# Kernel optimization log

Measured on AMD Instinct MI355X. Metric: run time of the kernel, lower is better.

Reference implementation:

```python
import jax, jax.numpy as jnp
import numpy as np

N, H, W, C, G, K = 8, 64, 64, 128, 8, 3
GC = C // G          # group channels = 16
P = K * K            # 9 sampling points
PAD = DIL = STRIDE = 1
OS = 1.0             # offset_scale
EPS = 1e-6
H_IN, W_IN = H + 2 * PAD, W + 2 * PAD


def _grid_sample_nhwc(img, grid):
    # img: (B, Hi, Wi, Cc) ; grid: (B, L, Pp, 2) in [-1,1]
    # bilinear, padding_mode='zeros', align_corners=False (matches F.grid_sample)
    B, Hi, Wi, Cc = img.shape
    gx = (grid[..., 0] + 1.0) * (Wi * 0.5) - 0.5
    gy = (grid[..., 1] + 1.0) * (Hi * 0.5) - 0.5
    x0 = jnp.floor(gx)
    y0 = jnp.floor(gy)
    wx1 = gx - x0
    wy1 = gy - y0
    b = jnp.arange(B).reshape(B, 1, 1)

    def tap(xi, yi, wgt):
        valid = (xi >= 0) & (xi <= Wi - 1) & (yi >= 0) & (yi <= Hi - 1)
        xc = jnp.clip(xi, 0, Wi - 1).astype(jnp.int32)
        yc = jnp.clip(yi, 0, Hi - 1).astype(jnp.int32)
        return img[b, yc, xc] * (wgt * valid)[..., None]

    return (tap(x0, y0, (1 - wx1) * (1 - wy1))
            + tap(x0 + 1, y0, wx1 * (1 - wy1))
            + tap(x0, y0 + 1, (1 - wx1) * wy1)
            + tap(x0 + 1, y0 + 1, wx1 * wy1))


def _forward(x, w_in, b_in, dw_w, dw_b, ln_g, ln_b, w_off, b_off, w_msk, b_msk, w_out, b_out):
    n = x.shape[0]
    x_proj = x @ w_in + b_in                                  # input_proj (n,H,W,C)
    # dw_conv: depthwise 3x3 -> LayerNorm(channels_last) -> GELU
    x1 = jax.lax.conv_general_dilated(
        x, dw_w, (1, 1), [((K - 1) // 2,) * 2] * 2,
        dimension_numbers=('NHWC', 'HWIO', 'NHWC'), feature_group_count=C) + dw_b
    mu = jnp.mean(x1, -1, keepdims=True)
    var = jnp.mean((x1 - mu) ** 2, -1, keepdims=True)
    x1 = (x1 - mu) * jax.lax.rsqrt(var + EPS) * ln_g + ln_b
    x1 = jax.nn.gelu(x1, approximate=False)
    offset = x1 @ w_off + b_off                               # (n,H,W,G*P*2)
    mask = jax.nn.softmax((x1 @ w_msk + b_msk).reshape(n, H, W, G, P), axis=-1)
    # reference points on the padded input (pixel-center, normalized)
    ry = (DIL * (K - 1) // 2 + 0.5 + jnp.arange(H, dtype=jnp.float32) * STRIDE) / H_IN
    rx = (DIL * (K - 1) // 2 + 0.5 + jnp.arange(W, dtype=jnp.float32) * STRIDE) / W_IN
    ref = jnp.stack([jnp.broadcast_to(rx[None, :], (H, W)),
                     jnp.broadcast_to(ry[:, None], (H, W))], -1)      # (H,W,2) = (x,y)
    # dilation kernel grid, x-major flatten (matches torch meshgrid indexing='ij')
    ks = jnp.arange(K, dtype=jnp.float32) * DIL - DIL * (K - 1) // 2
    gxk, gyk = jnp.meshgrid(ks, ks, indexing='ij')
    pts = jnp.stack([gxk / W_IN, gyk / H_IN], -1).reshape(P, 2)
    pts = jnp.tile(pts, (G, 1))                                       # (G*P,2), group-major
    loc = (ref[:, :, None, :] + pts[None, None, :, :] * OS).reshape(1, H, W, G * P * 2)
    snorm = jnp.tile(jnp.array([W_IN, H_IN], jnp.float32), G * P)     # [w,h,w,h,...]
    loc = loc + offset * OS / snorm
    grids = (2.0 * loc - 1.0).reshape(n, H * W, G, P, 2)
    grids = grids.transpose(0, 2, 1, 3, 4).reshape(n * G, H * W, P, 2)
    x_pad = jnp.pad(x_proj, ((0, 0), (PAD, PAD), (PAD, PAD), (0, 0)))
    img = x_pad.reshape(n, H_IN, W_IN, G, GC).transpose(0, 3, 1, 2, 4).reshape(n * G, H_IN, W_IN, GC)
    sampled = _grid_sample_nhwc(img, grids)                            # (n*G, HW, P, GC)
    m = mask.reshape(n, H * W, G, P).transpose(0, 2, 1, 3).reshape(n * G, H * W, P)
    out = (sampled * m[..., None]).sum(2)                              # (n*G, HW, GC)
    out = out.reshape(n, G, H * W, GC).transpose(0, 2, 1, 3).reshape(n, H, W, C)
    return out @ w_out + b_out                                         # output_proj


def setup_inputs():
    key = jax.random.key(0)
    k = jax.random.split(key, 8)
    s = 0.02
    f = jnp.float32
    return {
        'x': jax.random.normal(k[0], (N, H, W, C), f),
        'w_in': jax.random.normal(k[1], (C, C), f) * (1.0 / np.sqrt(C)),
        'b_in': jnp.zeros((C,), f),
        'dw_w': jax.random.normal(k[2], (K, K, 1, C), f) * s,
        'dw_b': jnp.zeros((C,), f),
        'ln_g': jnp.ones((C,), f),
        'ln_b': jnp.zeros((C,), f),
        'w_off': jax.random.normal(k[3], (C, G * P * 2), f) * s,
        'b_off': jax.random.normal(k[4], (G * P * 2,), f) * s,
        'w_msk': jax.random.normal(k[5], (C, G * P), f) * s,
        'b_msk': jnp.zeros((G * P,), f),
        'w_out': jax.random.normal(k[6], (C, C), f) * (1.0 / np.sqrt(C)),
        'b_out': jnp.zeros((C,), f),
    }


def reference(x, w_in, b_in, dw_w, dw_b, ln_g, ln_b, w_off, b_off, w_msk, b_msk, w_out, b_out):
    return _forward(x, w_in, b_in, dw_w, dw_b, ln_g, ln_b, w_off, b_off, w_msk, b_msk, w_out, b_out)
```

## Files before the change

### kernel.cpp

```cpp
#include <hip/hip_runtime.h>
#include <math.h>

#define NB 8
#define H 64
#define W 64
#define C 128
#define G 8
#define GC 16
#define P 9
#define NPIX (NB * H * W)
#define N_OFF 144
#define N_MSK 72
#define PXB 32
#define RECW 232
#define PK_IN_ELEMS   (8 * 4 * 64 * 8)
#define PK_COMB_ELEMS (14 * 4 * 64 * 8)
#define PK_OUT_ELEMS  (8 * 4 * 64 * 8)

using bf16x8 = __attribute__((ext_vector_type(8))) short;
using f32x4  = __attribute__((ext_vector_type(4))) float;
using u32x4  = __attribute__((ext_vector_type(4))) unsigned;

__device__ __forceinline__ short f2bf(float f) {
    union { float fv; unsigned u; } v; v.fv = f;
    unsigned r = v.u + 0x7fffu + ((v.u >> 16) & 1u);
    return (short)(r >> 16);
}

__global__ __launch_bounds__(256) void k_pack(
    const float* __restrict__ w_in, const float* __restrict__ w_off,
    const float* __restrict__ w_msk, const float* __restrict__ w_out,
    short* __restrict__ pk_in, short* __restrict__ pk_comb, short* __restrict__ pk_out)
{
    const int tid = blockIdx.x * 256 + threadIdx.x;
    int p, which;
    if (tid < PK_IN_ELEMS) { p = tid; which = 0; }
    else if (tid < PK_IN_ELEMS + PK_COMB_ELEMS) { p = tid - PK_IN_ELEMS; which = 1; }
    else if (tid < PK_IN_ELEMS + PK_COMB_ELEMS + PK_OUT_ELEMS) { p = tid - PK_IN_ELEMS - PK_COMB_ELEMS; which = 2; }
    else return;
    const int e = p & 7, lane = (p >> 3) & 63, kt = (p >> 9) & 3, nt = p >> 11;
    const int k = kt * 32 + (lane >> 4) * 8 + e;
    const int n = nt * 16 + (lane & 15);
    float v;
    if (which == 0) {
        v = w_in[k * C + n];
        pk_in[p] = f2bf(v);
    } else if (which == 1) {
        if (n < N_OFF) v = w_off[k * N_OFF + n];
        else if (n < N_OFF + N_MSK) v = w_msk[k * N_MSK + (n - N_OFF)];
        else v = 0.f;
        pk_comb[p] = f2bf(v);
    } else {
        v = w_out[k * C + n];
        pk_out[p] = f2bf(v);
    }
}

__global__ __launch_bounds__(256, 2) void k_fm(
    const float* __restrict__ x, const float* __restrict__ dw_w,
    const float* __restrict__ dw_b, const float* __restrict__ ln_g,
    const float* __restrict__ ln_b, const short* __restrict__ pk_in,
    const float* __restrict__ b_in, const short* __restrict__ pk_comb,
    const float* __restrict__ b_off, const float* __restrict__ b_msk,
    unsigned short* __restrict__ xproj, float* __restrict__ out)
{
    __shared__ __align__(16) short xa[PXB * C];
    __shared__ __align__(16) short x1s[PXB * C];
    __shared__ unsigned short recs[PXB * RECW];

    const int t = threadIdx.x;
    const int n = blockIdx.x & 7;
    const int local = blockIdx.x >> 3;
    const int y = local >> 1;
    const int xb = (local & 1) * PXB;
    const int gpix0 = (n * H + y) * W + xb;

    const int px = t >> 3;
    const int c8 = t & 7;
    const int cb = c8 * 4;
    const int gpx = gpix0 + px;
    const int sw = (px & 7) << 4;

    float a[16];
    #pragma unroll
    for (int q = 0; q < 4; ++q) {
        f32x4 v = *(const f32x4*)(dw_b + cb + q * 32);
        #pragma unroll
        for (int e = 0; e < 4; ++e) a[q * 4 + e] = v[e];
    }
    #pragma unroll
    for (int ky = 0; ky < 3; ++ky) {
        const int yy = y + ky - 1;
        if (yy < 0 || yy >= H) continue;
        #pragma unroll
        for (int kx = 0; kx < 3; ++kx) {
            const int xx = xb + px + kx - 1;
            if (xx < 0 || xx >= W) continue;
            const float* xp = x + ((size_t)(n * H + yy) * W + xx) * C;
            const float* wp = dw_w + (ky * 3 + kx) * C;
            #pragma unroll
            for (int q = 0; q < 4; ++q) {
                f32x4 xv = *(const f32x4*)(xp + cb + q * 32);
                f32x4 wv = *(const f32x4*)(wp + cb + q * 32);
                #pragma unroll
                for (int e = 0; e < 4; ++e)
                    a[q * 4 + e] = fmaf(xv[e], wv[e], a[q * 4 + e]);
            }
        }
    }
    {
        const float* cp = x + (size_t)gpx * C;
        #pragma unroll
        for (int q = 0; q < 4; ++q) {
            f32x4 v = *(const f32x4*)(cp + cb + q * 32);
            const unsigned lo = ((unsigned)(unsigned short)f2bf(v[0])) |
                                (((unsigned)(unsigned short)f2bf(v[1])) << 16);
            const unsigned hi = ((unsigned)(unsigned short)f2bf(v[2])) |
                                (((unsigned)(unsigned short)f2bf(v[3])) << 16);
            *(unsigned long long*)((char*)xa + px * 256 + ((cb * 2 + q * 64) ^ sw)) =
                ((unsigned long long)hi << 32) | lo;
        }
    }
    float mu, rsg;
    {
        float s = 0.f, sq = 0.f;
        #pragma unroll
        for (int cc = 0; cc < 16; ++cc) { s += a[cc]; sq = fmaf(a[cc], a[cc], sq); }
        #pragma unroll
        for (int d = 1; d < 8; d <<= 1) {
            s += __shfl_xor(s, d);
            sq += __shfl_xor(sq, d);
        }
        mu = s * (1.f / C);
        const float va = sq * (1.f / C) - mu * mu;
        rsg = rsqrtf(va + 1e-6f);
    }
    #pragma unroll
    for (int q = 0; q < 4; ++q) {
        f32x4 gv = *(const f32x4*)(ln_g + cb + q * 32);
        f32x4 bv = *(const f32x4*)(ln_b + cb + q * 32);
        unsigned short h4[4];
        #pragma unroll
        for (int e = 0; e < 4; ++e) {
            float v = (a[q * 4 + e] - mu) * rsg * gv[e] + bv[e];
            h4[e] = (unsigned short)f2bf(v * 0.5f * (1.f + erff(v * 0.70710678118654752f)));
        }
        const unsigned lo = ((unsigned)h4[0]) | (((unsigned)h4[1]) << 16);
        const unsigned hi = ((unsigned)h4[2]) | (((unsigned)h4[3]) << 16);
        *(unsigned long long*)((char*)x1s + px * 256 + ((cb * 2 + q * 64) ^ sw)) =
            ((unsigned long long)hi << 32) | lo;
    }
    __syncthreads();

    {
        const int w = t >> 6, l = t & 63;
        const int swA = (l & 7) << 4;
        bf16x8 aA[2][4], aB[2][4];
        #pragma unroll
        for (int mt = 0; mt < 2; ++mt) {
            const int m = mt * 16 + (l & 15);
            #pragma unroll
            for (int kt = 0; kt < 4; ++kt) {
                const int byte = m * 256 + ((kt * 64 + (l >> 4) * 16) ^ swA);
                aA[mt][kt] = *(const bf16x8*)((char*)xa + byte);
                aB[mt][kt] = *(const bf16x8*)((char*)x1s + byte);
            }
        }
        #pragma unroll
        for (int i = 0; i < 2; ++i) {
            const int nt = w + i * 4;
            bf16x8 bf[4];
            const short* bp = pk_in + nt * 2048 + l * 8;
            #pragma unroll
            for (int kt = 0; kt < 4; ++kt) bf[kt] = *(const bf16x8*)(bp + kt * 512);
            const float bias = b_in[nt * 16 + (l & 15)];
            #pragma unroll
            for (int mt = 0; mt < 2; ++mt) {
                f32x4 acc = {0.f, 0.f, 0.f, 0.f};
                #pragma unroll
                for (int kt = 0; kt < 4; ++kt)
                    acc = __builtin_amdgcn_mfma_f32_16x16x32_bf16(aA[mt][kt], bf[kt], acc, 0, 0, 0);
                const int prow = gpix0 + mt * 16 + (l >> 4) * 4;
                #pragma unroll
                for (int r = 0; r < 4; ++r)
                    xproj[(size_t)(nt * NPIX + prow + r) * 16 + (l & 15)] =
                        (unsigned short)f2bf(acc[r] + bias);
            }
        }
        #pragma unroll
        for (int i = 0; i < 4; ++i) {
            const int nt = w + i * 4;
            if (nt < 14) {
                bf16x8 bf[4];
                const short* bp = pk_comb + nt * 2048 + l * 8;
                #pragma unroll
                for (int kt = 0; kt < 4; ++kt) bf[kt] = *(const bf16x8*)(bp + kt * 512);
                const int col = nt * 16 + (l & 15);
                int dcol = col;
                float bias = 0.f;
                bool valid = true;
                if (col < N_OFF) bias = b_off[col];
                else {
                    const int cm = col - N_OFF;
                    if (cm < N_MSK) {
                        const int g = (cm * 57) >> 9;
                        dcol = 144 + g * 10 + (cm - 9 * g);
                        bias = b_msk[cm];
                    } else valid = false;
                }
                #pragma unroll
                for (int mt = 0; mt < 2; ++mt) {
                    f32x4 acc = {0.f, 0.f, 0.f, 0.f};
                    #pragma unroll
                    for (int kt = 0; kt < 4; ++kt)
                        acc = __builtin_amdgcn_mfma_f32_16x16x32_bf16(aB[mt][kt], bf[kt], acc, 0, 0, 0);
                    if (valid) {
                        const int pr0 = mt * 16 + (l >> 4) * 4;
                        #pragma unroll
                        for (int r = 0; r < 4; ++r)
                            recs[(pr0 + r) * RECW + dcol] = (unsigned short)f2bf(acc[r] + bias);
                    }
                }
            }
        }
    }
    __syncthreads();

    {
        const int spx = t >> 3, g = t & 7;
        unsigned short* row = recs + spx * RECW + 144 + g * 10;
        float lg[P];
        #pragma unroll
        for (int p = 0; p < P; ++p) lg[p] = __uint_as_float(((unsigned)row[p]) << 16);
        float mx = lg[0];
        #pragma unroll
        for (int p2 = 1; p2 < P; ++p2) mx = fmaxf(mx, lg[p2]);
        float e[P], s = 0.f;
        #pragma unroll
        for (int p2 = 0; p2 < P; ++p2) { e[p2] = expf(lg[p2] - mx); s += e[p2]; }
        const float inv = 1.0f / s;
        #pragma unroll
        for (int p2 = 0; p2 < P; ++p2) row[p2] = (unsigned short)f2bf(e[p2] * inv);
    }
    __syncthreads();

    {
        const int spx = t >> 3, q0 = t & 7;
        const char* srcL = (const char*)recs + spx * (RECW * 2);
        char* dst = (char*)out + (size_t)(gpix0 + spx) * 512;
        #pragma unroll
        for (int h = 0; h < 4; ++h) {
            const int q = q0 + h * 8;
            if (q < 28)
                *(bf16x8*)(dst + q * 16) = *(const bf16x8*)(srcL + q * 16);
        }
    }
}

#define PADX 41
__global__ __launch_bounds__(256, 2) void k_samp(
    const unsigned short* __restrict__ xproj, const short* __restrict__ pk_out,
    const float* __restrict__ b_out, float* __restrict__ out)
{
    __shared__ __align__(16) short smp[PXB * C];
    __shared__ __align__(16) u32x4 win[2 * 4 * 5 * PADX];

    const int t = threadIdx.x;
    const int n = blockIdx.x & 7;
    const int local = blockIdx.x >> 3;
    const int y = local >> 1;
    const int xb = (local & 1) * PXB;
    const int gpix0 = (n * H + y) * W + xb;
    const int imgbase = n * (H * W);

    const int spx = t & 31;
    const int gl = (t >> 5) & 3;
    const int half = t >> 7;
    const int xabs = xb + spx;
    const int swz = (spx & 7) << 4;
    const unsigned* slot = (const unsigned*)((const char*)out +
                           (size_t)(gpix0 + spx) * 512);

    for (int f = 0; f < 2; ++f) {
        const int g = f * 4 + gl;

        float cf[25];
        #pragma unroll
        for (int i = 0; i < 25; ++i) cf[i] = 0.f;
        float amax = 0.f;
        {
            u32x4 a0 = *(const u32x4*)(slot + g * 9);
            u32x4 a1 = *(const u32x4*)(slot + g * 9 + 4);
            const unsigned ov8 = slot[g * 9 + 8];
            u32x4 b0 = *(const u32x4*)(slot + 72 + 5 * g);
            const unsigned pb4 = slot[72 + 5 * g + 4];
            #pragma unroll
            for (int p = 0; p < P; ++p) {
                const unsigned ovp = (p < 4) ? a0[p & 3] : (p < 8) ? a1[p & 3] : ov8;
                const unsigned pu = (p < 8) ? b0[p >> 1] : pb4;
                const float m = (p & 1) ? __uint_as_float(pu & 0xffff0000u)
                                        : __uint_as_float(pu << 16);
                const float ox = __uint_as_float(ovp << 16);
                const float oy = __uint_as_float(ovp & 0xffff0000u);
                amax = fmaxf(amax, fmaxf(fabsf(ox), fabsf(oy)));
                const float fx = floorf(ox);
                const float fy = floorf(oy);
                const float wx = ox - fx, wy = oy - fy;
                const bool lox = fx < -0.5f;
                const bool loy = fy < -0.5f;
                const float wc0 = lox ? (1.f - wx) : 0.f;
                const float wc1 = lox ? wx : (1.f - wx);
                const float wc2 = lox ? 0.f : wx;
                const float wr0 = loy ? (1.f - wy) : 0.f;
                const float wr1 = loy ? wy : (1.f - wy);
                const float wr2 = loy ? 0.f : wy;
                const float mr0 = m * wr0, mr1 = m * wr1, mr2 = m * wr2;
                const int dxp = p / 3 - 1, dyp = p % 3 - 1;
                const int base = (dyp + 1) * 5 + (dxp + 1);
                cf[base + 0]  = fmaf(wc0, mr0, cf[base + 0]);
                cf[base + 1]  = fmaf(wc1, mr0, cf[base + 1]);
                cf[base + 2]  = fmaf(wc2, mr0, cf[base + 2]);
                cf[base + 5]  = fmaf(wc0, mr1, cf[base + 5]);
                cf[base + 6]  = fmaf(wc1, mr1, cf[base + 6]);
                cf[base + 7]  = fmaf(wc2, mr1, cf[base + 7]);
                cf[base + 10] = fmaf(wc0, mr2, cf[base + 10]);
                cf[base + 11] = fmaf(wc1, mr2, cf[base + 11]);
                cf[base + 12] = fmaf(wc2, mr2, cf[base + 12]);
            }
        }
        #pragma unroll
        for (int j = 0; j < 5; ++j) {
            const int xc = xabs + j - 2;
            if (!((xc >= 0) & (xc < W))) {
                #pragma unroll
                for (int i = 0; i < 5; ++i) cf[i * 5 + j] = 0.f;
            }
        }
        #pragma unroll
        for (int i = 0; i < 5; ++i) {
            const int yc = y + i - 2;
            if (!((yc >= 0) & (yc < H))) {
                #pragma unroll
                for (int j = 0; j < 5; ++j) cf[i * 5 + j] = 0.f;
            }
        }
        __syncthreads();

        for (int e = t; e < 1600; e += 256) {
            const int uh = e & 1;
            const int v = e >> 1;
            const int xs = v % 40;
            const int q2 = v / 40;
            const int rs = q2 % 5;
            const int gs = q2 / 5;
            const int row = min(max(y - 2 + rs, 0), H - 1);
            const int col = min(max(xb - 4 + xs, 0), W - 1);
            win[((uh * 4 + gs) * 5 + rs) * PADX + xs] =
                *(const u32x4*)(xproj +
                    ((size_t)((f * 4 + gs) * NPIX + imgbase + row * W + col)) * 16 + uh * 8);
        }
        __syncthreads();

        {
            float acc[8];
            #pragma unroll
            for (int q = 0; q < 8; ++q) acc[q] = 0.f;
            if (amax < 1.0f) {
                const u32x4* wb = win + (half * 4 + gl) * 5 * PADX + spx + 2;
                #pragma unroll
                for (int rr = 0; rr < 5; ++rr) {
                    #pragma unroll
                    for (int cc = 0; cc < 5; ++cc) {
                        const float c = cf[rr * 5 + cc];
                        const u32x4 v = wb[rr * PADX + cc];
                        #pragma unroll
                        for (int e = 0; e < 4; ++e) {
                            acc[2 * e]     = fmaf(c, __uint_as_float(v[e] << 16), acc[2 * e]);
                            acc[2 * e + 1] = fmaf(c, __uint_as_float(v[e] & 0xffff0000u), acc[2 * e + 1]);
                        }
                    }
                }
            } else {
                const u32x4* plane4 = (const u32x4*)(xproj + (size_t)(g * NPIX + imgbase) * 16);
                for (int p = 0; p < P; ++p) {
                    const unsigned ovp = slot[g * 9 + p];
                    const unsigned pu = slot[72 + 5 * g + (p >> 1)];
                    const float m = (p & 1) ? __uint_as_float(pu & 0xffff0000u)
                                            : __uint_as_float(pu << 16);
                    const float ux = (float)(xabs + (p / 3) - 1) + __uint_as_float(ovp << 16);
                    const float uy = (float)(y + (p % 3) - 1) + __uint_as_float(ovp & 0xffff0000u);
                    const float fx = floorf(ux), fy = floorf(uy);
                    const float wx = ux - fx, wy = uy - fy;
                    const int x0 = (int)fx, y0 = (int)fy;
                    float w4[4];
                    w4[0] = m * (1.f - wx) * (1.f - wy);
                    w4[1] = m * wx * (1.f - wy);
                    w4[2] = m * (1.f - wx) * wy;
                    w4[3] = m * wx * wy;
                    if (!((x0 >= 0) & (x0 < W)))       { w4[0] = 0.f; w4[2] = 0.f; }
                    if (!((x0 >= -1) & (x0 < W - 1)))  { w4[1] = 0.f; w4[3] = 0.f; }
                    if (!((y0 >= 0) & (y0 < H)))       { w4[0] = 0.f; w4[1] = 0.f; }
                    if (!((y0 >= -1) & (y0 < H - 1)))  { w4[2] = 0.f; w4[3] = 0.f; }
                    const int xc[2] = { min(max(x0, 0), W - 1), min(max(x0 + 1, 0), W - 1) };
                    const int yc[2] = { min(max(y0, 0), H - 1), min(max(y0 + 1, 0), H - 1) };
                    for (int cn = 0; cn < 4; ++cn) {
                        const float wgt = w4[cn];
                        if (wgt == 0.f) continue;
                        const u32x4 v = plane4[(size_t)(yc[cn >> 1] * W + xc[cn & 1]) * 2 + half];
                        #pragma unroll
                        for (int e = 0; e < 4; ++e) {
                            acc[2 * e]     = fmaf(wgt, __uint_as_float(v[e] << 16), acc[2 * e]);
                            acc[2 * e + 1] = fmaf(wgt, __uint_as_float(v[e] & 0xffff0000u), acc[2 * e + 1]);
                        }
                    }
                }
            }
            bf16x8 pk;
            #pragma unroll
            for (int e = 0; e < 8; ++e) pk[e] = f2bf(acc[e]);
            *(bf16x8*)((char*)smp + spx * 256 + ((g * 32 + half * 16) ^ swz)) = pk;
        }
    }
    __syncthreads();

    {
        const int w = t >> 6, l = t & 63;
        const int swA = (l & 7) << 4;
        bf16x8 aS[2][4];
        #pragma unroll
        for (int mt = 0; mt < 2; ++mt) {
            const int m = mt * 16 + (l & 15);
            #pragma unroll
            for (int kt = 0; kt < 4; ++kt)
                aS[mt][kt] = *(const bf16x8*)((char*)smp + m * 256 +
                                              ((kt * 64 + (l >> 4) * 16) ^ swA));
        }
        #pragma unroll
        for (int i = 0; i < 2; ++i) {
            const int nt = w + i * 4;
            bf16x8 bf[4];
            const short* bp = pk_out + nt * 2048 + l * 8;
            #pragma unroll
            for (int kt = 0; kt < 4; ++kt) bf[kt] = *(const bf16x8*)(bp + kt * 512);
            const float bias = b_out[nt * 16 + (l & 15)];
            #pragma unroll
            for (int mt = 0; mt < 2; ++mt) {
                f32x4 acc2 = {0.f, 0.f, 0.f, 0.f};
                #pragma unroll
                for (int kt = 0; kt < 4; ++kt)
                    acc2 = __builtin_amdgcn_mfma_f32_16x16x32_bf16(aS[mt][kt], bf[kt], acc2, 0, 0, 0);
                const int row0 = gpix0 + mt * 16 + (l >> 4) * 4;
                #pragma unroll
                for (int r = 0; r < 4; ++r)
                    out[(size_t)(row0 + r) * C + nt * 16 + (l & 15)] = acc2[r] + bias;
            }
        }
    }
}

extern "C" void kernel_launch(void* const* d_in, const int* in_sizes, int n_in,
                              void* d_out, int out_size, void* d_ws, size_t ws_size,
                              hipStream_t stream)
{
    const float* x     = (const float*)d_in[0];
    const float* w_in  = (const float*)d_in[1];
    const float* b_in  = (const float*)d_in[2];
    const float* dw_w  = (const float*)d_in[3];
    const float* dw_b  = (const float*)d_in[4];
    const float* ln_g  = (const float*)d_in[5];
    const float* ln_b  = (const float*)d_in[6];
    const float* w_off = (const float*)d_in[7];
    const float* b_off = (const float*)d_in[8];
    const float* w_msk = (const float*)d_in[9];
    const float* b_msk = (const float*)d_in[10];
    const float* w_out = (const float*)d_in[11];
    const float* b_out = (const float*)d_in[12];

    short* pk_in   = (short*)d_ws;
    short* pk_comb = pk_in + PK_IN_ELEMS;
    short* pk_out  = pk_comb + PK_COMB_ELEMS;
    unsigned short* xproj = (unsigned short*)(pk_out + PK_OUT_ELEMS);
    float* out     = (float*)d_out;

    hipLaunchKernelGGL(k_pack, dim3(240), dim3(256), 0, stream,
                       w_in, w_off, w_msk, w_out, pk_in, pk_comb, pk_out);
    hipLaunchKernelGGL(k_fm, dim3(NPIX / PXB), dim3(256), 0, stream,
                       x, dw_w, dw_b, ln_g, ln_b, pk_in, b_in,
                       pk_comb, b_off, b_msk, xproj, out);
    hipLaunchKernelGGL(k_samp, dim3(NPIX / PXB), dim3(256), 0, stream,
                       xproj, pk_out, b_out, out);
}
```

Measured before the change: 50.46 us.

## Split input projection into front kernel and fuse offset/mask with sampling and output

```diff
diff --git a/kernel.cpp b/kernel.cpp
--- a/kernel.cpp
+++ b/kernel.cpp
@@ -56,18 +56,10 @@
     }
 }
 
-__global__ __launch_bounds__(256, 2) void k_fm(
-    const float* __restrict__ x, const float* __restrict__ dw_w,
-    const float* __restrict__ dw_b, const float* __restrict__ ln_g,
-    const float* __restrict__ ln_b, const short* __restrict__ pk_in,
-    const float* __restrict__ b_in, const short* __restrict__ pk_comb,
-    const float* __restrict__ b_off, const float* __restrict__ b_msk,
-    unsigned short* __restrict__ xproj, float* __restrict__ out)
+__global__ __launch_bounds__(256, 2) void k_front(
+    const float* __restrict__ x, const short* __restrict__ pk_in,
+    const float* __restrict__ b_in, unsigned short* __restrict__ xproj)
 {
-    __shared__ __align__(16) short xa[PXB * C];
-    __shared__ __align__(16) short x1s[PXB * C];
-    __shared__ unsigned short recs[PXB * RECW];
-
     const int t = threadIdx.x;
     const int n = blockIdx.x & 7;
     const int local = blockIdx.x >> 3;
@@ -75,10 +67,67 @@
     const int xb = (local & 1) * PXB;
     const int gpix0 = (n * H + y) * W + xb;
 
+    const int w = t >> 6, l = t & 63;
+    bf16x8 aA[2][4];
+    #pragma unroll
+    for (int mt = 0; mt < 2; ++mt) {
+        const int m = mt * 16 + (l & 15);
+        const float* rp = x + (size_t)(gpix0 + m) * C + (l >> 4) * 8;
+        #pragma unroll
+        for (int kt = 0; kt < 4; ++kt) {
+            f32x4 v0 = *(const f32x4*)(rp + kt * 32);
+            f32x4 v1 = *(const f32x4*)(rp + kt * 32 + 4);
+            bf16x8 pk;
+            #pragma unroll
+            for (int e = 0; e < 4; ++e) { pk[e] = f2bf(v0[e]); pk[4 + e] = f2bf(v1[e]); }
+            aA[mt][kt] = pk;
+        }
+    }
+    #pragma unroll
+    for (int i = 0; i < 2; ++i) {
+        const int nt = w + i * 4;
+        bf16x8 bf[4];
+        const short* bp = pk_in + nt * 2048 + l * 8;
+        #pragma unroll
+        for (int kt = 0; kt < 4; ++kt) bf[kt] = *(const bf16x8*)(bp + kt * 512);
+        const float bias = b_in[nt * 16 + (l & 15)];
+        #pragma unroll
+        for (int mt = 0; mt < 2; ++mt) {
+            f32x4 acc = {0.f, 0.f, 0.f, 0.f};
+            #pragma unroll
+            for (int kt = 0; kt < 4; ++kt)
+                acc = __builtin_amdgcn_mfma_f32_16x16x32_bf16(aA[mt][kt], bf[kt], acc, 0, 0, 0);
+            const int prow = gpix0 + mt * 16 + (l >> 4) * 4;
+            #pragma unroll
+            for (int r = 0; r < 4; ++r)
+                xproj[(size_t)(nt * NPIX + prow + r) * 16 + (l & 15)] =
+                    (unsigned short)f2bf(acc[r] + bias);
+        }
+    }
+}
+
+__global__ __launch_bounds__(256, 2) void k_back(
+    const float* __restrict__ x, const float* __restrict__ dw_w,
+    const float* __restrict__ dw_b, const float* __restrict__ ln_g,
+    const float* __restrict__ ln_b, const short* __restrict__ pk_comb,
+    const float* __restrict__ b_off, const float* __restrict__ b_msk,
+    const unsigned short* __restrict__ xproj, const short* __restrict__ pk_out,
+    const float* __restrict__ b_out, float* __restrict__ out)
+{
+    __shared__ __align__(16) short buf0[PXB * C];
+    __shared__ unsigned short recs[PXB * RECW];
+
+    const int t = threadIdx.x;
+    const int n = blockIdx.x & 7;
+    const int local = blockIdx.x >> 3;
+    const int y = local >> 1;
+    const int xb = (local & 1) * PXB;
+    const int gpix0 = (n * H + y) * W + xb;
+    const int imgbase = n * (H * W);
+
     const int px = t >> 3;
     const int c8 = t & 7;
     const int cb = c8 * 4;
-    const int gpx = gpix0 + px;
     const int sw = (px & 7) << 4;
 
     float a[16];
@@ -108,19 +157,6 @@
             }
         }
     }
-    {
-        const float* cp = x + (size_t)gpx * C;
-        #pragma unroll
-        for (int q = 0; q < 4; ++q) {
-            f32x4 v = *(const f32x4*)(cp + cb + q * 32);
-            const unsigned lo = ((unsigned)(unsigned short)f2bf(v[0])) |
-                                (((unsigned)(unsigned short)f2bf(v[1])) << 16);
-            const unsigned hi = ((unsigned)(unsigned short)f2bf(v[2])) |
-                                (((unsigned)(unsigned short)f2bf(v[3])) << 16);
-            *(unsigned long long*)((char*)xa + px * 256 + ((cb * 2 + q * 64) ^ sw)) =
-                ((unsigned long long)hi << 32) | lo;
-        }
-    }
     float mu, rsg;
     {
         float s = 0.f, sq = 0.f;
@@ -131,8 +167,8 @@
             s += __shfl_xor(s, d);
             sq += __shfl_xor(sq, d);
         }
-        mu = s * (1.f / C);
-        const float va = sq * (1.f / C) - mu * mu;
+        mu = s * (1.0f / C);
+        const float va = sq * (1.0f / C) - mu * mu;
         rsg = rsqrtf(va + 1e-6f);
     }
     #pragma unroll
@@ -147,7 +183,7 @@
         }
         const unsigned lo = ((unsigned)h4[0]) | (((unsigned)h4[1]) << 16);
         const unsigned hi = ((unsigned)h4[2]) | (((unsigned)h4[3]) << 16);
-        *(unsigned long long*)((char*)x1s + px * 256 + ((cb * 2 + q * 64) ^ sw)) =
+        *(unsigned long long*)((char*)buf0 + px * 256 + ((cb * 2 + q * 64) ^ sw)) =
             ((unsigned long long)hi << 32) | lo;
     }
     __syncthreads();
@@ -155,37 +191,14 @@
     {
         const int w = t >> 6, l = t & 63;
         const int swA = (l & 7) << 4;
-        bf16x8 aA[2][4], aB[2][4];
+        bf16x8 aB[2][4];
         #pragma unroll
         for (int mt = 0; mt < 2; ++mt) {
             const int m = mt * 16 + (l & 15);
             #pragma unroll
-            for (int kt = 0; kt < 4; ++kt) {
-                const int byte = m * 256 + ((kt * 64 + (l >> 4) * 16) ^ swA);
-                aA[mt][kt] = *(const bf16x8*)((char*)xa + byte);
-                aB[mt][kt] = *(const bf16x8*)((char*)x1s + byte);
-            }
-        }
-        #pragma unroll
-        for (int i = 0; i < 2; ++i) {
-            const int nt = w + i * 4;
-            bf16x8 bf[4];
-            const short* bp = pk_in + nt * 2048 + l * 8;
-            #pragma unroll
-            for (int kt = 0; kt < 4; ++kt) bf[kt] = *(const bf16x8*)(bp + kt * 512);
-            const float bias = b_in[nt * 16 + (l & 15)];
-            #pragma unroll
-            for (int mt = 0; mt < 2; ++mt) {
-                f32x4 acc = {0.f, 0.f, 0.f, 0.f};
-                #pragma unroll
-                for (int kt = 0; kt < 4; ++kt)
-                    acc = __builtin_amdgcn_mfma_f32_16x16x32_bf16(aA[mt][kt], bf[kt], acc, 0, 0, 0);
-                const int prow = gpix0 + mt * 16 + (l >> 4) * 4;
-                #pragma unroll
-                for (int r = 0; r < 4; ++r)
-                    xproj[(size_t)(nt * NPIX + prow + r) * 16 + (l & 15)] =
-                        (unsigned short)f2bf(acc[r] + bias);
-            }
+            for (int kt = 0; kt < 4; ++kt)
+                aB[mt][kt] = *(const bf16x8*)((char*)buf0 + m * 256 +
+                                              ((kt * 64 + (l >> 4) * 16) ^ swA));
         }
         #pragma unroll
         for (int i = 0; i < 4; ++i) {
@@ -245,88 +258,45 @@
     __syncthreads();
 
     {
-        const int spx = t >> 3, q0 = t & 7;
-        const char* srcL = (const char*)recs + spx * (RECW * 2);
-        char* dst = (char*)out + (size_t)(gpix0 + spx) * 512;
-        #pragma unroll
-        for (int h = 0; h < 4; ++h) {
-            const int q = q0 + h * 8;
-            if (q < 28)
-                *(bf16x8*)(dst + q * 16) = *(const bf16x8*)(srcL + q * 16);
-        }
-    }
-}
-
-#define PADX 41
-__global__ __launch_bounds__(256, 2) void k_samp(
-    const unsigned short* __restrict__ xproj, const short* __restrict__ pk_out,
-    const float* __restrict__ b_out, float* __restrict__ out)
-{
-    __shared__ __align__(16) short smp[PXB * C];
-    __shared__ __align__(16) u32x4 win[2 * 4 * 5 * PADX];
-
-    const int t = threadIdx.x;
-    const int n = blockIdx.x & 7;
-    const int local = blockIdx.x >> 3;
-    const int y = local >> 1;
-    const int xb = (local & 1) * PXB;
-    const int gpix0 = (n * H + y) * W + xb;
-    const int imgbase = n * (H * W);
-
-    const int spx = t & 31;
-    const int gl = (t >> 5) & 3;
-    const int half = t >> 7;
-    const int xabs = xb + spx;
-    const int swz = (spx & 7) << 4;
-    const unsigned* slot = (const unsigned*)((const char*)out +
-                           (size_t)(gpix0 + spx) * 512);
-
-    for (int f = 0; f < 2; ++f) {
-        const int g = f * 4 + gl;
+        const int spx = t & 31, g = t >> 5;
+        const int xabs = xb + spx;
+        const int swz = (spx & 7) << 4;
+        const unsigned* rec32 = (const unsigned*)recs + spx * (RECW / 2);
+        const unsigned short* prp = recs + spx * RECW + 144 + g * 10;
 
         float cf[25];
         #pragma unroll
         for (int i = 0; i < 25; ++i) cf[i] = 0.f;
         float amax = 0.f;
-        {
-            u32x4 a0 = *(const u32x4*)(slot + g * 9);
-            u32x4 a1 = *(const u32x4*)(slot + g * 9 + 4);
-            const unsigned ov8 = slot[g * 9 + 8];
-            u32x4 b0 = *(const u32x4*)(slot + 72 + 5 * g);
-            const unsigned pb4 = slot[72 + 5 * g + 4];
-            #pragma unroll
-            for (int p = 0; p < P; ++p) {
-                const unsigned ovp = (p < 4) ? a0[p & 3] : (p < 8) ? a1[p & 3] : ov8;
-                const unsigned pu = (p < 8) ? b0[p >> 1] : pb4;
-                const float m = (p & 1) ? __uint_as_float(pu & 0xffff0000u)
-                                        : __uint_as_float(pu << 16);
-                const float ox = __uint_as_float(ovp << 16);
-                const float oy = __uint_as_float(ovp & 0xffff0000u);
-                amax = fmaxf(amax, fmaxf(fabsf(ox), fabsf(oy)));
-                const float fx = floorf(ox);
-                const float fy = floorf(oy);
-                const float wx = ox - fx, wy = oy - fy;
-                const bool lox = fx < -0.5f;
-                const bool loy = fy < -0.5f;
-                const float wc0 = lox ? (1.f - wx) : 0.f;
-                const float wc1 = lox ? wx : (1.f - wx);
-                const float wc2 = lox ? 0.f : wx;
-                const float wr0 = loy ? (1.f - wy) : 0.f;
-                const float wr1 = loy ? wy : (1.f - wy);
-                const float wr2 = loy ? 0.f : wy;
-                const float mr0 = m * wr0, mr1 = m * wr1, mr2 = m * wr2;
-                const int dxp = p / 3 - 1, dyp = p % 3 - 1;
-                const int base = (dyp + 1) * 5 + (dxp + 1);
-                cf[base + 0]  = fmaf(wc0, mr0, cf[base + 0]);
-                cf[base + 1]  = fmaf(wc1, mr0, cf[base + 1]);
-                cf[base + 2]  = fmaf(wc2, mr0, cf[base + 2]);
-                cf[base + 5]  = fmaf(wc0, mr1, cf[base + 5]);
-                cf[base + 6]  = fmaf(wc1, mr1, cf[base + 6]);
-                cf[base + 7]  = fmaf(wc2, mr1, cf[base + 7]);
-                cf[base + 10] = fmaf(wc0, mr2, cf[base + 10]);
-                cf[base + 11] = fmaf(wc1, mr2, cf[base + 11]);
-                cf[base + 12] = fmaf(wc2, mr2, cf[base + 12]);
-            }
+        #pragma unroll
+        for (int p = 0; p < P; ++p) {
+            const unsigned ovp = rec32[g * 9 + p];
+            const float m = __uint_as_float(((unsigned)prp[p]) << 16);
+            const float ox = __uint_as_float(ovp << 16);
+            const float oy = __uint_as_float(ovp & 0xffff0000u);
+            amax = fmaxf(amax, fmaxf(fabsf(ox), fabsf(oy)));
+            const float fx = floorf(ox);
+            const float fy = floorf(oy);
+            const float wx = ox - fx, wy = oy - fy;
+            const bool lox = fx < -0.5f;
+            const bool loy = fy < -0.5f;
+            const float wc0 = lox ? (1.f - wx) : 0.f;
+            const float wc1 = lox ? wx : (1.f - wx);
+            const float wc2 = lox ? 0.f : wx;
+            const float wr0 = loy ? (1.f - wy) : 0.f;
+            const float wr1 = loy ? wy : (1.f - wy);
+            const float wr2 = loy ? 0.f : wy;
+            const float mr0 = m * wr0, mr1 = m * wr1, mr2 = m * wr2;
+            const int base = (p % 3) * 5 + (p / 3);
+            cf[base + 0]  = fmaf(wc0, mr0, cf[base + 0]);
+            cf[base + 1]  = fmaf(wc1, mr0, cf[base + 1]);
+            cf[base + 2]  = fmaf(wc2, mr0, cf[base + 2]);
+            cf[base + 5]  = fmaf(wc0, mr1, cf[base + 5]);
+            cf[base + 6]  = fmaf(wc1, mr1, cf[base + 6]);
+            cf[base + 7]  = fmaf(wc2, mr1, cf[base + 7]);
+            cf[base + 10] = fmaf(wc0, mr2, cf[base + 10]);
+            cf[base + 11] = fmaf(wc1, mr2, cf[base + 11]);
+            cf[base + 12] = fmaf(wc2, mr2, cf[base + 12]);
         }
         #pragma unroll
         for (int j = 0; j < 5; ++j) {
@@ -344,81 +314,79 @@
                 for (int j = 0; j < 5; ++j) cf[i * 5 + j] = 0.f;
             }
         }
-        __syncthreads();
-
-        for (int e = t; e < 1600; e += 256) {
-            const int uh = e & 1;
-            const int v = e >> 1;
-            const int xs = v % 40;
-            const int q2 = v / 40;
-            const int rs = q2 % 5;
-            const int gs = q2 / 5;
-            const int row = min(max(y - 2 + rs, 0), H - 1);
-            const int col = min(max(xb - 4 + xs, 0), W - 1);
-            win[((uh * 4 + gs) * 5 + rs) * PADX + xs] =
-                *(const u32x4*)(xproj +
-                    ((size_t)((f * 4 + gs) * NPIX + imgbase + row * W + col)) * 16 + uh * 8);
-        }
-        __syncthreads();
-
-        {
-            float acc[8];
-            #pragma unroll
-            for (int q = 0; q < 8; ++q) acc[q] = 0.f;
-            if (amax < 1.0f) {
-                const u32x4* wb = win + (half * 4 + gl) * 5 * PADX + spx + 2;
-                #pragma unroll
-                for (int rr = 0; rr < 5; ++rr) {
+        const char* pb = (const char*)(xproj + (size_t)(g * NPIX + imgbase) * 16);
+        int rowoff[5], coloff[5];
+        #pragma unroll
+        for (int i = 0; i < 5; ++i) {
+            rowoff[i] = min(max(y + i - 2, 0), H - 1) * (W * 32);
+            coloff[i] = min(max(xabs + i - 2, 0), W - 1) * 32;
+        }
+
+        float acc[16];
+        #pragma unroll
+        for (int q = 0; q < 16; ++q) acc[q] = 0.f;
+
+        if (amax < 1.0f) {
+            #pragma unroll
+            for (int i = 0; i < 5; ++i) {
+                #pragma unroll
+                for (int j = 0; j < 5; ++j) {
+                    const float c = cf[i * 5 + j];
+                    const char* ap = pb + (rowoff[i] + coloff[j]);
+                    u32x4 v0 = *(const u32x4*)ap;
+                    u32x4 v1 = *(const u32x4*)(ap + 16);
                     #pragma unroll
-                    for (int cc = 0; cc < 5; ++cc) {
-                        const float c = cf[rr * 5 + cc];
-                        const u32x4 v = wb[rr * PADX + cc];
-                        #pragma unroll
-                        for (int e = 0; e < 4; ++e) {
-                            acc[2 * e]     = fmaf(c, __uint_as_float(v[e] << 16), acc[2 * e]);
-                            acc[2 * e + 1] = fmaf(c, __uint_as_float(v[e] & 0xffff0000u), acc[2 * e + 1]);
-                        }
+                    for (int e = 0; e < 4; ++e) {
+                        acc[2 * e]         = fmaf(c, __uint_as_float(v0[e] << 16), acc[2 * e]);
+                        acc[2 * e + 1]     = fmaf(c, __uint_as_float(v0[e] & 0xffff0000u), acc[2 * e + 1]);
+                        acc[8 + 2 * e]     = fmaf(c, __uint_as_float(v1[e] << 16), acc[8 + 2 * e]);
+                        acc[8 + 2 * e + 1] = fmaf(c, __uint_as_float(v1[e] & 0xffff0000u), acc[8 + 2 * e + 1]);
                     }
                 }
-            } else {
-                const u32x4* plane4 = (const u32x4*)(xproj + (size_t)(g * NPIX + imgbase) * 16);
-                for (int p = 0; p < P; ++p) {
-                    const unsigned ovp = slot[g * 9 + p];
-                    const unsigned pu = slot[72 + 5 * g + (p >> 1)];
-                    const float m = (p & 1) ? __uint_as_float(pu & 0xffff0000u)
-                                            : __uint_as_float(pu << 16);
-                    const float ux = (float)(xabs + (p / 3) - 1) + __uint_as_float(ovp << 16);
-                    const float uy = (float)(y + (p % 3) - 1) + __uint_as_float(ovp & 0xffff0000u);
-                    const float fx = floorf(ux), fy = floorf(uy);
-                    const float wx = ux - fx, wy = uy - fy;
-                    const int x0 = (int)fx, y0 = (int)fy;
-                    float w4[4];
-                    w4[0] = m * (1.f - wx) * (1.f - wy);
-                    w4[1] = m * wx * (1.f - wy);
-                    w4[2] = m * (1.f - wx) * wy;
-                    w4[3] = m * wx * wy;
-                    if (!((x0 >= 0) & (x0 < W)))       { w4[0] = 0.f; w4[2] = 0.f; }
-                    if (!((x0 >= -1) & (x0 < W - 1)))  { w4[1] = 0.f; w4[3] = 0.f; }
-                    if (!((y0 >= 0) & (y0 < H)))       { w4[0] = 0.f; w4[1] = 0.f; }
-                    if (!((y0 >= -1) & (y0 < H - 1)))  { w4[2] = 0.f; w4[3] = 0.f; }
-                    const int xc[2] = { min(max(x0, 0), W - 1), min(max(x0 + 1, 0), W - 1) };
-                    const int yc[2] = { min(max(y0, 0), H - 1), min(max(y0 + 1, 0), H - 1) };
-                    for (int cn = 0; cn < 4; ++cn) {
-                        const float wgt = w4[cn];
-                        if (wgt == 0.f) continue;
-                        const u32x4 v = plane4[(size_t)(yc[cn >> 1] * W + xc[cn & 1]) * 2 + half];
-                        #pragma unroll
-                        for (int e = 0; e < 4; ++e) {
-                            acc[2 * e]     = fmaf(wgt, __uint_as_float(v[e] << 16), acc[2 * e]);
-                            acc[2 * e + 1] = fmaf(wgt, __uint_as_float(v[e] & 0xffff0000u), acc[2 * e + 1]);
-                        }
+            }
+        } else {
+            for (int p = 0; p < P; ++p) {
+                const unsigned ovp = rec32[g * 9 + p];
+                const float m = __uint_as_float(((unsigned)prp[p]) << 16);
+                const float ux = (float)(xabs + (p / 3) - 1) + __uint_as_float(ovp << 16);
+                const float uy = (float)(y + (p % 3) - 1) + __uint_as_float(ovp & 0xffff0000u);
+                const float fx = floorf(ux), fy = floorf(uy);
+                const float wx = ux - fx, wy = uy - fy;
+                const int x0 = (int)fx, y0 = (int)fy;
+                float w4[4];
+                w4[0] = m * (1.f - wx) * (1.f - wy);
+                w4[1] = m * wx * (1.f - wy);
+                w4[2] = m * (1.f - wx) * wy;
+                w4[3] = m * wx * wy;
+                if (!((x0 >= 0) & (x0 < W)))       { w4[0] = 0.f; w4[2] = 0.f; }
+                if (!((x0 >= -1) & (x0 < W - 1)))  { w4[1] = 0.f; w4[3] = 0.f; }
+                if (!((y0 >= 0) & (y0 < H)))       { w4[0] = 0.f; w4[1] = 0.f; }
+                if (!((y0 >= -1) & (y0 < H - 1)))  { w4[2] = 0.f; w4[3] = 0.f; }
+                const int xc[2] = { min(max(x0, 0), W - 1), min(max(x0 + 1, 0), W - 1) };
+                const int yc[2] = { min(max(y0, 0), H - 1), min(max(y0 + 1, 0), H - 1) };
+                for (int cn = 0; cn < 4; ++cn) {
+                    const float wgt = w4[cn];
+                    if (wgt == 0.f) continue;
+                    const char* ap = pb + ((size_t)(yc[cn >> 1] * W + xc[cn & 1]) * 32);
+                    u32x4 v0 = *(const u32x4*)ap;
+                    u32x4 v1 = *(const u32x4*)(ap + 16);
+                    #pragma unroll
+                    for (int e = 0; e < 4; ++e) {
+                        acc[2 * e]         = fmaf(wgt, __uint_as_float(v0[e] << 16), acc[2 * e]);
+                        acc[2 * e + 1]     = fmaf(wgt, __uint_as_float(v0[e] & 0xffff0000u), acc[2 * e + 1]);
+                        acc[8 + 2 * e]     = fmaf(wgt, __uint_as_float(v1[e] << 16), acc[8 + 2 * e]);
+                        acc[8 + 2 * e + 1] = fmaf(wgt, __uint_as_float(v1[e] & 0xffff0000u), acc[8 + 2 * e + 1]);
                     }
                 }
             }
+        }
+        __syncthreads();
+        #pragma unroll
+        for (int h = 0; h < 2; ++h) {
             bf16x8 pk;
             #pragma unroll
-            for (int e = 0; e < 8; ++e) pk[e] = f2bf(acc[e]);
-            *(bf16x8*)((char*)smp + spx * 256 + ((g * 32 + half * 16) ^ swz)) = pk;
+            for (int e = 0; e < 8; ++e) pk[e] = f2bf(acc[h * 8 + e]);
+            *(bf16x8*)((char*)buf0 + spx * 256 + ((g * 32 + h * 16) ^ swz)) = pk;
         }
     }
     __syncthreads();
@@ -432,7 +400,7 @@
             const int m = mt * 16 + (l & 15);
             #pragma unroll
             for (int kt = 0; kt < 4; ++kt)
-                aS[mt][kt] = *(const bf16x8*)((char*)smp + m * 256 +
+                aS[mt][kt] = *(const bf16x8*)((char*)buf0 + m * 256 +
                                               ((kt * 64 + (l >> 4) * 16) ^ swA));
         }
         #pragma unroll
@@ -484,9 +452,9 @@
 
     hipLaunchKernelGGL(k_pack, dim3(240), dim3(256), 0, stream,
                        w_in, w_off, w_msk, w_out, pk_in, pk_comb, pk_out);
-    hipLaunchKernelGGL(k_fm, dim3(NPIX / PXB), dim3(256), 0, stream,
-                       x, dw_w, dw_b, ln_g, ln_b, pk_in, b_in,
-                       pk_comb, b_off, b_msk, xproj, out);
-    hipLaunchKernelGGL(k_samp, dim3(NPIX / PXB), dim3(256), 0, stream,
+    hipLaunchKernelGGL(k_front, dim3(NPIX / PXB), dim3(256), 0, stream,
+                       x, pk_in, b_in, xproj);
+    hipLaunchKernelGGL(k_back, dim3(NPIX / PXB), dim3(256), 0, stream,
+                       x, dw_w, dw_b, ln_g, ln_b, pk_comb, b_off, b_msk,
                        xproj, pk_out, b_out, out);
 }
```

Result: slower. 52.76 us (+4.5%).
